# Optimization experiments

Hardware: AMD Instinct MI355X
Metric: run time of the kernel (lower is better)

Reference implementation:

```python
import jax, jax.numpy as jnp
import numpy as np

EMBED = 1024
HEADS = 16
HEAD_DIM = EMBED // HEADS

def setup_inputs() -> dict:
    key = jax.random.key(0)
    ks = jax.random.split(key, 5)
    B, S = 2, 2048
    scale = 1.0 / np.sqrt(EMBED)
    return {
        "query": jax.random.normal(ks[0], (B, S, EMBED), dtype=jnp.float32),
        "w_qkv": jax.random.normal(ks[1], (3 * EMBED, EMBED), dtype=jnp.float32) * scale,
        "b_qkv": jax.random.normal(ks[2], (3 * EMBED,), dtype=jnp.float32) * 0.01,
        "w_out": jax.random.normal(ks[3], (EMBED, EMBED), dtype=jnp.float32) * scale,
        "b_out": jax.random.normal(ks[4], (EMBED,), dtype=jnp.float32) * 0.01,
    }

def reference(query, w_qkv, b_qkv, w_out, b_out):
    B, S, E = query.shape
    H, D = HEADS, HEAD_DIM
    # fused qkv projection (torch Linear: x @ W.T + b)
    qkv = query @ w_qkv.T + b_qkv          # [B, S, 3E]
    q, k, v = jnp.split(qkv, 3, axis=-1)   # each [B, S, E]
    def heads(x):
        return x.reshape(B, S, H, D).transpose(0, 2, 1, 3)  # [B, H, S, D]
    q, k, v = heads(q), heads(k), heads(v)
    scale = D ** -0.5
    energy = jnp.einsum('bhqd,bhkd->bhqk', q, k) * scale    # [B, H, S, S]
    attn = jax.nn.softmax(energy, axis=-1)
    # dropout: inference mode (identity)
    out = jnp.einsum('bhqk,bhkd->bhqd', attn, v)            # [B, H, S, D]
    out = out.transpose(0, 2, 1, 3).reshape(B, S, E)
    return out @ w_out.T + b_out
```

## Files before the change

### kernel.cpp

```cpp
#include <hip/hip_runtime.h>
#include <hip/hip_bf16.h>
#include <cstdint>
#include <cstddef>


typedef float f32x4 __attribute__((ext_vector_type(4)));
typedef short s16x8 __attribute__((ext_vector_type(8)));

#define AS1C(p) ((const __attribute__((address_space(1))) void*)(p))
#define AS3(p)  ((__attribute__((address_space(3))) void*)(p))

__device__ __forceinline__ unsigned short f2bf(float f) {
    union { float f; unsigned u; } v; v.f = f;
    return (unsigned short)((v.u + 0x7FFFu + ((v.u >> 16) & 1u)) >> 16);
}

__device__ __forceinline__ float fast_exp2(float x) {
#if __has_builtin(__builtin_amdgcn_exp2f)
    return __builtin_amdgcn_exp2f(x);
#else
    return exp2f(x);
#endif
}

__global__ void cvt_bf16(const float* __restrict__ src,
                         unsigned short* __restrict__ dst, int n4) {
    int i = blockIdx.x * blockDim.x + threadIdx.x;
    if (i >= n4) return;
    float4 f = reinterpret_cast<const float4*>(src)[i];
    ushort4 o;
    o.x = f2bf(f.x); o.y = f2bf(f.y); o.z = f2bf(f.z); o.w = f2bf(f.w);
    reinterpret_cast<ushort4*>(dst)[i] = o;
}

#define QSCALE_L2E (0.125f * 1.44269504088896f)

template <int MODE>
__global__ __launch_bounds__(256, 2)
void gemm_bt(const unsigned short* __restrict__ A,
             const unsigned short* __restrict__ B,
             const float* __restrict__ bias,
             float* __restrict__ Cf,
             unsigned short* __restrict__ Qw,
             unsigned short* __restrict__ Kw,
             unsigned short* __restrict__ Vtw,
             int M, int N, int K) {
    constexpr int BK = 32;
    __shared__ unsigned short As[128 * BK];
    __shared__ unsigned short Bs[128 * BK];

    const int tid = threadIdx.x;
    const int wid = tid >> 6, lane = tid & 63;
    const int brow = blockIdx.y * 128, bcol = blockIdx.x * 128;
    const int wr = wid >> 1, wc = wid & 1;

    f32x4 acc[4][4] = {};

    const int kIters = K / BK;
    for (int kt = 0; kt < kIters; ++kt) {
#pragma unroll
        for (int i = 0; i < 2; ++i) {
            const int lb = (wid * 2 + i) * 1024;
            const int row = (lb >> 6) + (lane >> 2);
            const int inrow = (lane & 3) * 16;
            const char* ga = (const char*)A + ((size_t)(brow + row) * K + kt * BK) * 2 + inrow;
            __builtin_amdgcn_global_load_lds(AS1C(ga), AS3((char*)As + lb), 16, 0, 0);
            const char* gb = (const char*)B + ((size_t)(bcol + row) * K + kt * BK) * 2 + inrow;
            __builtin_amdgcn_global_load_lds(AS1C(gb), AS3((char*)Bs + lb), 16, 0, 0);
        }
        __syncthreads();

        s16x8 af[4], bfr[4];
#pragma unroll
        for (int f = 0; f < 4; ++f) {
            af[f]  = *(const s16x8*)((const char*)As + (wr * 64 + f * 16 + (lane & 15)) * 64 + (lane >> 4) * 16);
            bfr[f] = *(const s16x8*)((const char*)Bs + (wc * 64 + f * 16 + (lane & 15)) * 64 + (lane >> 4) * 16);
        }
#pragma unroll
        for (int mf = 0; mf < 4; ++mf)
#pragma unroll
            for (int nf = 0; nf < 4; ++nf)
                acc[mf][nf] = __builtin_amdgcn_mfma_f32_16x16x32_bf16(af[mf], bfr[nf], acc[mf][nf], 0, 0, 0);
        __syncthreads();
    }

    float bv[4];
#pragma unroll
    for (int nf = 0; nf < 4; ++nf) bv[nf] = bias[bcol + wc * 64 + nf * 16 + (lane & 15)];

#pragma unroll
    for (int mf = 0; mf < 4; ++mf) {
#pragma unroll
        for (int r = 0; r < 4; ++r) {
            const int row = brow + wr * 64 + mf * 16 + (lane >> 4) * 4 + r;
#pragma unroll
            for (int nf = 0; nf < 4; ++nf) {
                const int col = bcol + wc * 64 + nf * 16 + (lane & 15);
                float v = acc[mf][nf][r] + bv[nf];
                if constexpr (MODE == 0) {
                    const int which = col >> 10, e = col & 1023;
                    const int h = e >> 6, d = e & 63;
                    const int b = row >> 11, s = row & 2047;
                    const size_t bh = (size_t)(b * 16 + h);
                    if (which == 0)      Qw[(bh * 2048 + s) * 64 + d] = f2bf(v * QSCALE_L2E);
                    else if (which == 1) Kw[(bh * 2048 + s) * 64 + d] = f2bf(v);
                    else                 Vtw[(bh * 64 + d) * 2048 + s] = f2bf(v);
                } else {
                    Cf[(size_t)row * N + col] = v;
                }
            }
        }
    }
}

__global__ __launch_bounds__(256, 4)
void attn_fwd(const unsigned short* __restrict__ Q,
              const unsigned short* __restrict__ Kk,
              const unsigned short* __restrict__ Vt,
              unsigned short* __restrict__ O) {
    __shared__ unsigned short Ks[2][64 * 64];
    __shared__ unsigned short Vs[2][64 * 64];
    __shared__ unsigned short Ps[4 * 16 * 64];

    const int tid = threadIdx.x;
    const int wid = tid >> 6, lane = tid & 63;
    const int bh = blockIdx.y;
    const int b = bh >> 4, h = bh & 15;
    const int q0 = blockIdx.x * 64 + wid * 16;

    const char* Qb  = (const char*)(Q  + (size_t)bh * 2048 * 64);
    const char* Kb  = (const char*)(Kk + (size_t)bh * 2048 * 64);
    const char* Vtb = (const char*)(Vt + (size_t)bh * 64 * 2048);
    char* PsW = (char*)Ps + wid * 2048;

    s16x8 aq[2];
#pragma unroll
    for (int kf = 0; kf < 2; ++kf)
        aq[kf] = *(const s16x8*)(Qb + (size_t)(q0 + (lane & 15)) * 128 +
                                 (kf * 32 + (lane >> 4) * 8) * 2);

    f32x4 o_acc[4] = {};
    f32x4 l_acc = {};
    s16x8 ones;
#pragma unroll
    for (int j = 0; j < 8; ++j) ones[j] = (short)0x3F80;

    auto stage = [&](int kc, int buf) {
#pragma unroll
        for (int i = 0; i < 2; ++i) {
            const int lb = (wid * 2 + i) * 1024;
            const int row = (lb >> 7) + (lane >> 3);
            const int inrow = (lane & 7) * 16;
            const int srcin = inrow ^ ((row & 7) << 4);
            const char* gk = Kb + (size_t)(kc * 64 + row) * 128 + srcin;
            __builtin_amdgcn_global_load_lds(AS1C(gk), AS3((char*)Ks[buf] + lb), 16, 0, 0);
            const char* gv = Vtb + (size_t)row * 4096 + kc * 128 + srcin;
            __builtin_amdgcn_global_load_lds(AS1C(gv), AS3((char*)Vs[buf] + lb), 16, 0, 0);
        }
    };

    stage(0, 0);
    __syncthreads();

    for (int kc = 0; kc < 32; ++kc) {
        const int cur = kc & 1;
        if (kc < 31) stage(kc + 1, cur ^ 1);

        f32x4 sacc[4];
#pragma unroll
        for (int nf = 0; nf < 4; ++nf) sacc[nf] = f32x4{-16.f, -16.f, -16.f, -16.f};
#pragma unroll
        for (int kf = 0; kf < 2; ++kf) {
            s16x8 bk[4];
#pragma unroll
            for (int nf = 0; nf < 4; ++nf) {
                const int key = nf * 16 + (lane & 15);
                bk[nf] = *(const s16x8*)((const char*)Ks[cur] + key * 128 +
                                         (((kf * 32 + (lane >> 4) * 8) * 2) ^ ((key & 7) << 4)));
            }
#pragma unroll
            for (int nf = 0; nf < 4; ++nf)
                sacc[nf] = __builtin_amdgcn_mfma_f32_16x16x32_bf16(aq[kf], bk[nf], sacc[nf], 0, 0, 0);
        }

#pragma unroll
        for (int r = 0; r < 4; ++r) {
            const int prow = (lane >> 4) * 4 + r;
            char* pbase = PsW + prow * 128;
#pragma unroll
            for (int nf = 0; nf < 4; ++nf) {
                const float p = fast_exp2(sacc[nf][r]);
                const int cb = (nf * 16 + (lane & 15)) * 2;
                *(unsigned short*)(pbase + (cb ^ ((prow & 7) << 4))) = f2bf(p);
            }
        }

        s16x8 pa[2];
#pragma unroll
        for (int kf = 0; kf < 2; ++kf) {
            const int prow = lane & 15;
            pa[kf] = *(const s16x8*)(PsW + prow * 128 +
                                     (((kf * 32 + (lane >> 4) * 8) * 2) ^ ((prow & 7) << 4)));
        }
#pragma unroll
        for (int kf = 0; kf < 2; ++kf) {
            l_acc = __builtin_amdgcn_mfma_f32_16x16x32_bf16(pa[kf], ones, l_acc, 0, 0, 0);
            s16x8 bv[4];
#pragma unroll
            for (int df = 0; df < 4; ++df) {
                const int drow = df * 16 + (lane & 15);
                bv[df] = *(const s16x8*)((const char*)Vs[cur] + drow * 128 +
                                         (((kf * 32 + (lane >> 4) * 8) * 2) ^ ((drow & 7) << 4)));
            }
#pragma unroll
            for (int df = 0; df < 4; ++df)
                o_acc[df] = __builtin_amdgcn_mfma_f32_16x16x32_bf16(pa[kf], bv[df], o_acc[df], 0, 0, 0);
        }
        __syncthreads();
    }

    float inv[4];
#pragma unroll
    for (int r = 0; r < 4; ++r) inv[r] = 1.f / l_acc[r];
#pragma unroll
    for (int df = 0; df < 4; ++df) {
#pragma unroll
        for (int r = 0; r < 4; ++r) {
            const int srow = q0 + (lane >> 4) * 4 + r;
            const int dcol = df * 16 + (lane & 15);
            O[(size_t)(b * 2048 + srow) * 1024 + h * 64 + dcol] = f2bf(o_acc[df][r] * inv[r]);
        }
    }
}

extern "C" void kernel_launch(void* const* d_in, const int* in_sizes, int n_in,
                              void* d_out, int out_size, void* d_ws, size_t ws_size,
                              hipStream_t stream) {
    const float* query = (const float*)d_in[0];
    const float* w_qkv = (const float*)d_in[1];
    const float* b_qkv = (const float*)d_in[2];
    const float* w_out = (const float*)d_in[3];
    const float* b_out = (const float*)d_in[4];
    float* out = (float*)d_out;

    unsigned short* ws = (unsigned short*)d_ws;
    unsigned short* Xbf    = ws;
    unsigned short* Wqkvbf = Xbf + 4096 * 1024;
    unsigned short* Woutbf = Wqkvbf + 3072 * 1024;
    unsigned short* Qw     = Woutbf + 1024 * 1024;
    unsigned short* Kw     = Qw + 32 * 2048 * 64;
    unsigned short* Vtw    = Kw + 32 * 2048 * 64;
    unsigned short* Obf    = Vtw + 32 * 2048 * 64;

    cvt_bf16<<<(4096 * 1024 / 4 + 255) / 256, 256, 0, stream>>>(query, Xbf, 4096 * 1024 / 4);
    cvt_bf16<<<(3072 * 1024 / 4 + 255) / 256, 256, 0, stream>>>(w_qkv, Wqkvbf, 3072 * 1024 / 4);
    cvt_bf16<<<(1024 * 1024 / 4 + 255) / 256, 256, 0, stream>>>(w_out, Woutbf, 1024 * 1024 / 4);

    gemm_bt<0><<<dim3(3072 / 128, 4096 / 128), 256, 0, stream>>>(
        Xbf, Wqkvbf, b_qkv, nullptr, Qw, Kw, Vtw, 4096, 3072, 1024);

    attn_fwd<<<dim3(32, 32), 256, 0, stream>>>(Qw, Kw, Vtw, Obf);

    gemm_bt<1><<<dim3(1024 / 128, 4096 / 128), 256, 0, stream>>>(
        Obf, Woutbf, b_out, out, nullptr, nullptr, nullptr, 4096, 1024, 1024);
}
```

Measured before the change: 147.7 us.

## Merge bf16 conversions into one launch, swizzle attention blocks, transpose score MFMA

The three fp32-to-bf16 conversion kernels become one kernel that picks its source by index range, removing two launches. The attention grid becomes 1D with an XCD-aware swizzle so blocks sharing a head land on the same chiplet, aiming for better L2 reuse of K/V. The QK^T MFMA operands are swapped so each lane holds four consecutive keys of one query row, letting P be written to LDS as packed 8-byte stores instead of scattered 2-byte stores. The softmax still relies on the existing fixed -16 offset with no running max.

```diff
diff --git a/kernel.cpp b/kernel.cpp
--- a/kernel.cpp
+++ b/kernel.cpp
@@ -23,14 +23,23 @@
 #endif
 }
 
-__global__ void cvt_bf16(const float* __restrict__ src,
-                         unsigned short* __restrict__ dst, int n4) {
-    int i = blockIdx.x * blockDim.x + threadIdx.x;
-    if (i >= n4) return;
-    float4 f = reinterpret_cast<const float4*>(src)[i];
+__global__ void cvt_bf16_3(const float* __restrict__ a, const float* __restrict__ b,
+                           const float* __restrict__ c,
+                           unsigned short* __restrict__ oa, unsigned short* __restrict__ ob,
+                           unsigned short* __restrict__ oc,
+                           int na4, int nb4, int nc4) {
+    int j = blockIdx.x * blockDim.x + threadIdx.x;
+    const float* s; unsigned short* d;
+    if (j < na4) { s = a; d = oa; }
+    else {
+        j -= na4;
+        if (j < nb4) { s = b; d = ob; }
+        else { j -= nb4; if (j >= nc4) return; s = c; d = oc; }
+    }
+    float4 f = reinterpret_cast<const float4*>(s)[j];
     ushort4 o;
     o.x = f2bf(f.x); o.y = f2bf(f.y); o.z = f2bf(f.z); o.w = f2bf(f.w);
-    reinterpret_cast<ushort4*>(dst)[i] = o;
+    reinterpret_cast<ushort4*>(d)[j] = o;
 }
 
 #define QSCALE_L2E (0.125f * 1.44269504088896f)
@@ -124,20 +133,26 @@
 
     const int tid = threadIdx.x;
     const int wid = tid >> 6, lane = tid & 63;
-    const int bh = blockIdx.y;
+
+    const int bid = blockIdx.x;
+    const int swzb = (bid & 7) * 128 + (bid >> 3);
+    const int bh = swzb >> 5;
+    const int qt = swzb & 31;
     const int b = bh >> 4, h = bh & 15;
-    const int q0 = blockIdx.x * 64 + wid * 16;
+    const int q0 = qt * 64 + wid * 16;
 
     const char* Qb  = (const char*)(Q  + (size_t)bh * 2048 * 64);
     const char* Kb  = (const char*)(Kk + (size_t)bh * 2048 * 64);
     const char* Vtb = (const char*)(Vt + (size_t)bh * 64 * 2048);
     char* PsW = (char*)Ps + wid * 2048;
 
+    const int q = lane & 15, g = lane >> 4;
+    const int qswz = (q & 7) << 4;
+
     s16x8 aq[2];
 #pragma unroll
     for (int kf = 0; kf < 2; ++kf)
-        aq[kf] = *(const s16x8*)(Qb + (size_t)(q0 + (lane & 15)) * 128 +
-                                 (kf * 32 + (lane >> 4) * 8) * 2);
+        aq[kf] = *(const s16x8*)(Qb + (size_t)(q0 + q) * 128 + (kf * 32 + g * 8) * 2);
 
     f32x4 o_acc[4] = {};
     f32x4 l_acc = {};
@@ -174,43 +189,44 @@
             s16x8 bk[4];
 #pragma unroll
             for (int nf = 0; nf < 4; ++nf) {
-                const int key = nf * 16 + (lane & 15);
+                const int key = nf * 16 + q;
                 bk[nf] = *(const s16x8*)((const char*)Ks[cur] + key * 128 +
-                                         (((kf * 32 + (lane >> 4) * 8) * 2) ^ ((key & 7) << 4)));
+                                         (((kf * 32 + g * 8) * 2) ^ ((key & 7) << 4)));
             }
 #pragma unroll
             for (int nf = 0; nf < 4; ++nf)
-                sacc[nf] = __builtin_amdgcn_mfma_f32_16x16x32_bf16(aq[kf], bk[nf], sacc[nf], 0, 0, 0);
-        }
-
-#pragma unroll
-        for (int r = 0; r < 4; ++r) {
-            const int prow = (lane >> 4) * 4 + r;
-            char* pbase = PsW + prow * 128;
+                sacc[nf] = __builtin_amdgcn_mfma_f32_16x16x32_bf16(bk[nf], aq[kf], sacc[nf], 0, 0, 0);
+        }
+
+        {
+            char* pbase = PsW + q * 128;
 #pragma unroll
             for (int nf = 0; nf < 4; ++nf) {
-                const float p = fast_exp2(sacc[nf][r]);
-                const int cb = (nf * 16 + (lane & 15)) * 2;
-                *(unsigned short*)(pbase + (cb ^ ((prow & 7) << 4))) = f2bf(p);
+                float2 lo2 = make_float2(fast_exp2(sacc[nf][0]), fast_exp2(sacc[nf][1]));
+                float2 hi2 = make_float2(fast_exp2(sacc[nf][2]), fast_exp2(sacc[nf][3]));
+                __hip_bfloat162 plo = __float22bfloat162_rn(lo2);
+                __hip_bfloat162 phi = __float22bfloat162_rn(hi2);
+                uint2 w;
+                w.x = *(unsigned*)&plo;
+                w.y = *(unsigned*)&phi;
+                const int cb = (nf * 16 + 4 * g) * 2;
+                *(uint2*)(pbase + (cb ^ qswz)) = w;
             }
         }
 
         s16x8 pa[2];
 #pragma unroll
-        for (int kf = 0; kf < 2; ++kf) {
-            const int prow = lane & 15;
-            pa[kf] = *(const s16x8*)(PsW + prow * 128 +
-                                     (((kf * 32 + (lane >> 4) * 8) * 2) ^ ((prow & 7) << 4)));
-        }
+        for (int kf = 0; kf < 2; ++kf)
+            pa[kf] = *(const s16x8*)(PsW + q * 128 + (((kf * 32 + g * 8) * 2) ^ qswz));
 #pragma unroll
         for (int kf = 0; kf < 2; ++kf) {
             l_acc = __builtin_amdgcn_mfma_f32_16x16x32_bf16(pa[kf], ones, l_acc, 0, 0, 0);
             s16x8 bv[4];
 #pragma unroll
             for (int df = 0; df < 4; ++df) {
-                const int drow = df * 16 + (lane & 15);
+                const int drow = df * 16 + q;
                 bv[df] = *(const s16x8*)((const char*)Vs[cur] + drow * 128 +
-                                         (((kf * 32 + (lane >> 4) * 8) * 2) ^ ((drow & 7) << 4)));
+                                         (((kf * 32 + g * 8) * 2) ^ ((drow & 7) << 4)));
             }
 #pragma unroll
             for (int df = 0; df < 4; ++df)
@@ -226,8 +242,8 @@
     for (int df = 0; df < 4; ++df) {
 #pragma unroll
         for (int r = 0; r < 4; ++r) {
-            const int srow = q0 + (lane >> 4) * 4 + r;
-            const int dcol = df * 16 + (lane & 15);
+            const int srow = q0 + g * 4 + r;
+            const int dcol = df * 16 + q;
             O[(size_t)(b * 2048 + srow) * 1024 + h * 64 + dcol] = f2bf(o_acc[df][r] * inv[r]);
         }
     }
@@ -252,14 +268,14 @@
     unsigned short* Vtw    = Kw + 32 * 2048 * 64;
     unsigned short* Obf    = Vtw + 32 * 2048 * 64;
 
-    cvt_bf16<<<(4096 * 1024 / 4 + 255) / 256, 256, 0, stream>>>(query, Xbf, 4096 * 1024 / 4);
-    cvt_bf16<<<(3072 * 1024 / 4 + 255) / 256, 256, 0, stream>>>(w_qkv, Wqkvbf, 3072 * 1024 / 4);
-    cvt_bf16<<<(1024 * 1024 / 4 + 255) / 256, 256, 0, stream>>>(w_out, Woutbf, 1024 * 1024 / 4);
+    const int na4 = 4096 * 1024 / 4, nb4 = 3072 * 1024 / 4, nc4 = 1024 * 1024 / 4;
+    cvt_bf16_3<<<(na4 + nb4 + nc4 + 255) / 256, 256, 0, stream>>>(
+        query, w_qkv, w_out, Xbf, Wqkvbf, Woutbf, na4, nb4, nc4);
 
     gemm_bt<0><<<dim3(3072 / 128, 4096 / 128), 256, 0, stream>>>(
         Xbf, Wqkvbf, b_qkv, nullptr, Qw, Kw, Vtw, 4096, 3072, 1024);
 
-    attn_fwd<<<dim3(32, 32), 256, 0, stream>>>(Qw, Kw, Vtw, Obf);
+    attn_fwd<<<dim3(1024), 256, 0, stream>>>(Qw, Kw, Vtw, Obf);
 
     gemm_bt<1><<<dim3(1024 / 128, 4096 / 128), 256, 0, stream>>>(
         Obf, Woutbf, b_out, out, nullptr, nullptr, nullptr, 4096, 1024, 1024);
```

After: 132.5 us, median of 2. 1.12x faster.
